# Performance work log

Measured on AMD Instinct MI355X. Metric: run time of the kernel, lower is better.

## Reference

```python
import jax, jax.numpy as jnp
import numpy as np

B, S, D, H = 8, 1024, 1024, 16
DH = D // H  # 64
LN_EPS = 1e-5


def setup_inputs() -> dict:
    key = jax.random.key(0)
    ks = jax.random.split(key, 12)
    w = lambda k, shape: (jax.random.normal(k, shape, dtype=jnp.float32) * 0.02)
    return {
        "key": jax.random.normal(ks[0], (B, S, D), dtype=jnp.float32),
        "value": jax.random.normal(ks[1], (B, S, D), dtype=jnp.float32),
        "query": jax.random.normal(ks[2], (B, S, D), dtype=jnp.float32),
        "atten_mask": jax.random.randint(ks[3], (B, S, S), 0, 2).astype(bool),
        "Wk": w(ks[4], (D, D)), "bk": jnp.zeros((D,), jnp.float32),
        "Wv": w(ks[5], (D, D)), "bv": jnp.zeros((D,), jnp.float32),
        "Wq": w(ks[6], (D, D)), "bq": jnp.zeros((D,), jnp.float32),
        "Wf": w(ks[7], (D, D)), "bf": jnp.zeros((D,), jnp.float32),
        "gamma": jnp.ones((D,), jnp.float32),
        "beta": jnp.zeros((D,), jnp.float32),
    }


def reference(key, value, query, atten_mask, Wk, bk, Wv, bv, Wq, bq, Wf, bf, gamma, beta):
    residual = query
    k = key @ Wk + bk      # [B,S,D]
    v = value @ Wv + bv
    q = query @ Wq + bq
    # Faithful to the original: raw .view(B*H, -1, d) reshape, NO head transpose.
    k = k.reshape(B * H, S, DH)
    v = v.reshape(B * H, S, DH)
    q = q.reshape(B * H, S, DH)
    # torch .repeat(H,1,1) tiles along batch dim -> head bh uses mask[bh % B]
    mask = jnp.tile(atten_mask, (H, 1, 1))  # [B*H, S, S]
    scale = (DH // H) ** (-0.5)  # quirky original scaling: (64//16)**-0.5 = 0.5
    scores = jnp.einsum('bqd,bkd->bqk', q, k) * scale  # [B*H, S, S]
    scores = jnp.where(mask, jnp.float32(-1e6), scores)
    attention = jax.nn.softmax(scores, axis=2)
    context = jnp.einsum('bqk,bkd->bqd', attention, v)  # [B*H, S, DH]
    context = context.reshape(B, S, D)
    out = context @ Wf + bf
    out = residual + out
    # LayerNorm over last dim
    mu = jnp.mean(out, axis=-1, keepdims=True)
    var = jnp.var(out, axis=-1, keepdims=True)
    out = (out - mu) * jax.lax.rsqrt(var + LN_EPS) * gamma + beta
    return out, attention
```

## Files before the change

kernel.cpp:

```cpp
#include <hip/hip_runtime.h>


typedef unsigned short u16;
typedef unsigned long long u64;
typedef __attribute__((ext_vector_type(8))) short bf16x8;
typedef __attribute__((ext_vector_type(4))) float f32x4;

#define MFMA_BF16(a, b, c) __builtin_amdgcn_mfma_f32_16x16x32_bf16((a), (b), (c), 0, 0, 0)

__device__ __forceinline__ u16 f2bf(float f) {
  unsigned u = __float_as_uint(f);
  u += 0x7fffu + ((u >> 16) & 1u);
  return (u16)(u >> 16);
}
__device__ __forceinline__ float bf2f(u16 b) {
  return __uint_as_float(((unsigned)b) << 16);
}
__device__ __forceinline__ void gload_lds16(const u16* g, u16* l) {
  __builtin_amdgcn_global_load_lds(
      (const __attribute__((address_space(1))) void*)g,
      (__attribute__((address_space(3))) void*)l, 16, 0, 0);
}

static constexpr size_t MD = 8192ull * 1024ull;
static constexpr size_t DD = 1024ull * 1024ull;
static constexpr float SCL = 0.72134752044f;

__global__ __launch_bounds__(256) void cvt_k(const float* __restrict__ K,
                                             const float* __restrict__ V,
                                             const float* __restrict__ Q,
                                             u16* __restrict__ O) {
  const int z = blockIdx.z;
  const float* src = (z == 0) ? K : ((z == 1) ? V : Q);
  const size_t i = ((size_t)blockIdx.x * 256 + threadIdx.x) * 4;
  const float4 v = *reinterpret_cast<const float4*>(src + i);
  ushort4 o;
  o.x = f2bf(v.x); o.y = f2bf(v.y); o.z = f2bf(v.z); o.w = f2bf(v.w);
  *reinterpret_cast<ushort4*>(O + (size_t)z * MD + i) = o;
}

__global__ __launch_bounds__(256) void wt_k(const float* __restrict__ Wk,
                                            const float* __restrict__ Wv,
                                            const float* __restrict__ Wq,
                                            const float* __restrict__ Wf,
                                            u16* __restrict__ WT) {
  const int z = blockIdx.z;
  const float* W = (z == 0) ? Wk : ((z == 1) ? Wv : ((z == 2) ? Wq : Wf));
  __shared__ float tile[32][33];
  const int k0 = blockIdx.y * 32, n0 = blockIdx.x * 32;
  const int r = threadIdx.x >> 5, c = threadIdx.x & 31;
#pragma unroll
  for (int rr = r; rr < 32; rr += 8)
    tile[rr][c] = W[(size_t)(k0 + rr) * 1024 + n0 + c];
  __syncthreads();
#pragma unroll
  for (int rr = r; rr < 32; rr += 8)
    WT[(size_t)z * DD + (size_t)(n0 + rr) * 1024 + k0 + c] = f2bf(tile[c][rr]);
}

__global__ __launch_bounds__(256) void mb_k(const unsigned char* __restrict__ mask8,
                                            u64* __restrict__ mb) {
  __shared__ int mflag;
  if (threadIdx.x == 0) {
    const unsigned* mw = reinterpret_cast<const unsigned*>(mask8);
    int allW = 1;
    for (int i = 0; i < 64; ++i) {
      const unsigned v = mw[i];
      if (v != 0u && v != 1u && v != 0x3F800000u) allW = 0;
    }
    mflag = allW;
  }
  __syncthreads();
  const int wide = mflag;
  const size_t wi = (size_t)blockIdx.x * 256 + threadIdx.x;
  const size_t src0 = wi * 64;
  u64 bits = 0ull;
  if (!wide) {
    const uint4* p = reinterpret_cast<const uint4*>(mask8 + src0);
#pragma unroll
    for (int q = 0; q < 4; ++q) {
      const uint4 v = p[q];
      const unsigned vv[4] = {v.x, v.y, v.z, v.w};
#pragma unroll
      for (int k = 0; k < 4; ++k) {
        unsigned tt = vv[k];
        tt |= tt >> 4; tt |= tt >> 2; tt |= tt >> 1;
        tt &= 0x01010101u;
        const unsigned nib =
            (tt & 1u) | ((tt >> 7) & 2u) | ((tt >> 14) & 4u) | ((tt >> 21) & 8u);
        bits |= (u64)nib << (q * 16 + k * 4);
      }
    }
  } else {
    const unsigned* p = reinterpret_cast<const unsigned*>(mask8) + src0;
#pragma unroll
    for (int k = 0; k < 64; ++k)
      bits |= (u64)(p[k] != 0u) << k;
  }
  mb[wi] = bits;
}

template <int EPI>
__global__ __launch_bounds__(256) void gemm_bt(
    const u16* __restrict__ A0, const u16* __restrict__ B0,
    const float* __restrict__ bias0, const float* __restrict__ bias1,
    const float* __restrict__ bias2, u16* __restrict__ Obf,
    float* __restrict__ Of, const float* __restrict__ resid) {
  __shared__ __align__(16) u16 As[128 * 32];
  __shared__ __align__(16) u16 Bs[128 * 32];
  const int z = blockIdx.z;
  const u16* A = A0 + (size_t)z * MD;
  const u16* Bt = B0 + (size_t)z * DD;
  const float* bias = (z == 0) ? bias0 : ((z == 1) ? bias1 : bias2);
  const int t = threadIdx.x;
  const int m0 = blockIdx.y * 128, n0 = blockIdx.x * 128;
  const int w = t >> 6, lane = t & 63, lr = lane & 15, lk = lane >> 4;
  const int wm = (w >> 1) * 64, wn = (w & 1) * 64;
  const int srow = lane >> 2, scol = (lane & 3) * 8;

  f32x4 acc[4][4] = {};

  for (int k0 = 0; k0 < 1024; k0 += 32) {
    __syncthreads();
#pragma unroll
    for (int it = 0; it < 2; ++it) {
      const int c = w * 2 + it;
      gload_lds16(A + (size_t)(m0 + 16 * c + srow) * 1024 + k0 + scol,
                  &As[c * 512 + lane * 8]);
      gload_lds16(Bt + (size_t)(n0 + 16 * c + srow) * 1024 + k0 + scol,
                  &Bs[c * 512 + lane * 8]);
    }
    __syncthreads();
    bf16x8 af[4], bfr[4];
#pragma unroll
    for (int i = 0; i < 4; ++i)
      af[i] = *reinterpret_cast<const bf16x8*>(&As[(wm + i * 16 + lr) * 32 + lk * 8]);
#pragma unroll
    for (int j = 0; j < 4; ++j)
      bfr[j] = *reinterpret_cast<const bf16x8*>(&Bs[(wn + j * 16 + lr) * 32 + lk * 8]);
#pragma unroll
    for (int i = 0; i < 4; ++i) {
#pragma unroll
      for (int j = 0; j < 4; ++j)
        acc[i][j] = MFMA_BF16(af[i], bfr[j], acc[i][j]);
    }
  }

#pragma unroll
  for (int i = 0; i < 4; ++i) {
#pragma unroll
    for (int j = 0; j < 4; ++j) {
#pragma unroll
      for (int r = 0; r < 4; ++r) {
        const int row = m0 + wm + i * 16 + lk * 4 + r;
        const int col = n0 + wn + j * 16 + lr;
        const float v = acc[i][j][r] + bias[col];
        if constexpr (EPI == 0) {
          Obf[(size_t)z * MD + (size_t)row * 1024 + col] = f2bf(v);
        } else {
          const size_t idx = (size_t)row * 1024 + col;
          Of[idx] = v + resid[idx];
        }
      }
    }
  }
}

__global__ __launch_bounds__(256) void vt_k(const u16* __restrict__ VP,
                                            u16* __restrict__ VTo) {
  __shared__ __align__(16) u16 tile[64][72];
  const int t = threadIdx.x;
  const int bh = blockIdx.y, p0 = blockIdx.x * 64;
  const int b = bh >> 4, shi = bh & 15;
  const size_t hb = (size_t)b * 1048576 + (size_t)shi * 65536;
#pragma unroll
  for (int it = 0; it < 2; ++it) {
    const int c = t + it * 256;
    const int row = c >> 3, f8 = (c & 7) * 8;
    const int p = p0 + row;
    *reinterpret_cast<int4*>(&tile[row][f8]) = *reinterpret_cast<const int4*>(
        VP + hb + (size_t)(p >> 4) * 1024 + (p & 15) * 64 + f8);
  }
  __syncthreads();
#pragma unroll
  for (int it = 0; it < 2; ++it) {
    const int c = t + it * 256;
    const int f = c >> 3, pc = (c & 7) * 8;
    __align__(16) u16 tmp[8];
#pragma unroll
    for (int i = 0; i < 8; ++i) tmp[i] = tile[pc + i][f];
    *reinterpret_cast<int4*>(VTo + (size_t)bh * 65536 + (size_t)f * 1024 + p0 + pc) =
        *reinterpret_cast<int4*>(tmp);
  }
}

__global__ __launch_bounds__(512, 4) void attn_k(
    const u16* __restrict__ QP, const u16* __restrict__ KP,
    const u16* __restrict__ VT, const u64* __restrict__ mb,
    float* __restrict__ attnOut, u16* __restrict__ ctx) {
  __shared__ __align__(16) u16 Ps[32 * 1024];
  __shared__ float red[8][2][16];

  const int t = threadIdx.x;
  const int qt = blockIdx.x;
  const int bh = blockIdx.y;
  const int q0 = qt * 32;
  const int b = bh >> 4, shi = bh & 15;
  const size_t hb = (size_t)b * 1048576 + (size_t)shi * 65536;
  const u64* mrow = mb + (size_t)(shi & 7) * 16384;

  const int w = t >> 6, lane = t & 63, lr = lane & 15, lk = lane >> 4;
  const int qsw = (lr & 7) << 3;

  bf16x8 qf[2][2];
#pragma unroll
  for (int rg = 0; rg < 2; ++rg) {
    const u16* qb = QP + hb + (size_t)(qt * 2 + rg) * 1024 + lr * 64 + lk * 8;
    qf[rg][0] = *reinterpret_cast<const bf16x8*>(qb);
    qf[rg][1] = *reinterpret_cast<const bf16x8*>(qb + 32);
  }

  float psum[2] = {0.f, 0.f};

#pragma unroll
  for (int ki = 0; ki < 2; ++ki) {
    const int kt = w * 2 + ki;
    const u16* kb = KP + hb + (size_t)(kt * 4) * 1024 + lr * 64 + lk * 8;
    bf16x8 kf[4][2];
#pragma unroll
    for (int j = 0; j < 4; ++j) {
      kf[j][0] = *reinterpret_cast<const bf16x8*>(kb + j * 1024);
      kf[j][1] = *reinterpret_cast<const bf16x8*>(kb + j * 1024 + 32);
    }
#pragma unroll
    for (int rg = 0; rg < 2; ++rg) {
      f32x4 sf[4];
#pragma unroll
      for (int j = 0; j < 4; ++j) {
        f32x4 a = {};
        a = MFMA_BF16(kf[j][0], qf[rg][0], a);
        a = MFMA_BF16(kf[j][1], qf[rg][1], a);
        sf[j] = a;
      }
      const u64 mw = mrow[(size_t)(q0 + rg * 16 + lr) * 16 + kt];
#pragma unroll
      for (int j = 0; j < 4; ++j) {
        u16 pb[4];
#pragma unroll
        for (int r = 0; r < 4; ++r) {
          const unsigned bit = (unsigned)(mw >> (j * 16 + lk * 4 + r)) & 1u;
          const float sel = bit ? -__builtin_inff() : 0.0f;
          const float p = __builtin_amdgcn_exp2f(fmaf(sf[j][r], SCL, sel));
          psum[rg] += p;
          pb[r] = f2bf(p);
        }
        const unsigned lo = (unsigned)pb[0] | ((unsigned)pb[1] << 16);
        const unsigned hi = (unsigned)pb[2] | ((unsigned)pb[3] << 16);
        const int kel = (kt * 64 + j * 16 + lk * 4) ^ qsw;
        *reinterpret_cast<u64*>(&Ps[(rg * 16 + lr) * 1024 + kel]) =
            (u64)lo | ((u64)hi << 32);
      }
    }
  }
#pragma unroll
  for (int rg = 0; rg < 2; ++rg) {
    psum[rg] += __shfl_xor(psum[rg], 16, 64);
    psum[rg] += __shfl_xor(psum[rg], 32, 64);
  }
  if (lane < 16) { red[w][0][lr] = psum[0]; red[w][1][lr] = psum[1]; }
  __syncthreads();

  const int rbase = (w >> 2) * 16, cg = (w & 3) * 16;
  const u16* vb = VT + (size_t)bh * 65536 + (size_t)(cg + lr) * 1024 + lk * 8;
  f32x4 cacc[4] = {};
#pragma unroll
  for (int kk = 0; kk < 32; ++kk) {
    const int kel = (kk * 32 + lk * 8) ^ qsw;
    const bf16x8 pf = *reinterpret_cast<const bf16x8*>(&Ps[(rbase + lr) * 1024 + kel]);
    const bf16x8 vf = *reinterpret_cast<const bf16x8*>(vb + kk * 32);
    cacc[kk & 3] = MFMA_BF16(pf, vf, cacc[kk & 3]);
  }
#pragma unroll
  for (int r = 0; r < 4; ++r) {
    const int l16 = lk * 4 + r;
    float rs = 0.f;
#pragma unroll
    for (int w2 = 0; w2 < 8; ++w2) rs += red[w2][w >> 2][l16];
    const float ri = (rs > 0.f) ? __builtin_amdgcn_rcpf(rs) : 0.f;
    const float cv = cacc[0][r] + cacc[1][r] + cacc[2][r] + cacc[3][r];
    const int p = q0 + rbase + l16;
    ctx[hb + (size_t)(p >> 4) * 1024 + (size_t)(p & 15) * 64 + cg + lr] = f2bf(cv * ri);
  }

  const int arow = t >> 4, ac4 = (t & 15) * 4;
  const int asw = (arow & 7) << 3;
  float rsA = 0.f;
#pragma unroll
  for (int w2 = 0; w2 < 8; ++w2) rsA += red[w2][arow >> 4][arow & 15];
  const float riA = (rsA > 0.f) ? __builtin_amdgcn_rcpf(rsA) : 0.f;
  float* aout = attnOut + (size_t)bh * 1048576 + (size_t)(q0 + arow) * 1024;
#pragma unroll
  for (int i = 0; i < 16; ++i) {
    const int col = i * 64 + ac4;
    const u64 p4 = *reinterpret_cast<const u64*>(&Ps[arow * 1024 + (col ^ asw)]);
    f32x4 o;
    o[0] = bf2f((u16)(p4 & 0xffffu)) * riA;
    o[1] = bf2f((u16)((p4 >> 16) & 0xffffu)) * riA;
    o[2] = bf2f((u16)((p4 >> 32) & 0xffffu)) * riA;
    o[3] = bf2f((u16)(p4 >> 48)) * riA;
    __builtin_nontemporal_store(o, reinterpret_cast<f32x4*>(aout + col));
  }
}

__global__ __launch_bounds__(256) void ln_k(const float* __restrict__ X,
                                            const float* __restrict__ gamma,
                                            const float* __restrict__ beta,
                                            float* __restrict__ Y) {
  const int row = blockIdx.x, t = threadIdx.x;
  const size_t base = (size_t)row * 1024;
  const float4 x = *reinterpret_cast<const float4*>(X + base + t * 4);
  float s = x.x + x.y + x.z + x.w;
  float s2 = x.x * x.x + x.y * x.y + x.z * x.z + x.w * x.w;
#pragma unroll
  for (int d = 1; d < 64; d <<= 1) {
    s += __shfl_xor(s, d, 64);
    s2 += __shfl_xor(s2, d, 64);
  }
  __shared__ float red[8];
  const int w = t >> 6;
  if ((t & 63) == 0) { red[w] = s; red[4 + w] = s2; }
  __syncthreads();
  s = red[0] + red[1] + red[2] + red[3];
  s2 = red[4] + red[5] + red[6] + red[7];
  const float mu = s * (1.f / 1024.f);
  const float var = s2 * (1.f / 1024.f) - mu * mu;
  const float inv = rsqrtf(var + 1e-5f);
  const float4 g = *reinterpret_cast<const float4*>(gamma + t * 4);
  const float4 be = *reinterpret_cast<const float4*>(beta + t * 4);
  float4 y;
  y.x = (x.x - mu) * inv * g.x + be.x;
  y.y = (x.y - mu) * inv * g.y + be.y;
  y.z = (x.z - mu) * inv * g.z + be.z;
  y.w = (x.w - mu) * inv * g.w + be.w;
  *reinterpret_cast<float4*>(Y + base + t * 4) = y;
}

extern "C" void kernel_launch(void* const* d_in, const int* in_sizes, int n_in,
                              void* d_out, int out_size, void* d_ws, size_t ws_size,
                              hipStream_t stream) {
  const float* keyF = (const float*)d_in[0];
  const float* valueF = (const float*)d_in[1];
  const float* queryF = (const float*)d_in[2];
  const unsigned char* mask8 = (const unsigned char*)d_in[3];
  const float* Wk = (const float*)d_in[4];
  const float* bk = (const float*)d_in[5];
  const float* Wv = (const float*)d_in[6];
  const float* bv = (const float*)d_in[7];
  const float* Wq = (const float*)d_in[8];
  const float* bq = (const float*)d_in[9];
  const float* Wf = (const float*)d_in[10];
  const float* bfp = (const float*)d_in[11];
  const float* gamma = (const float*)d_in[12];
  const float* beta = (const float*)d_in[13];

  char* ws = (char*)d_ws;
  u16* Xbf = (u16*)(ws);
  u16* WT = (u16*)(ws + 50331648);
  u16* KP = (u16*)(ws + 58720256);
  u16* VP = (u16*)(ws + 75497472);
  u16* QP = (u16*)(ws + 92274688);
  u16* VT = (u16*)(ws + 109051904);
  u64* MB = (u64*)(ws + 125829120);
  u16* CTX = (u16*)(ws);
  float* PRELN = (float*)(ws + 16777216);

  float* outF = (float*)d_out;
  float* attnF = outF + 8388608;

  cvt_k<<<dim3(8192, 1, 3), 256, 0, stream>>>(keyF, valueF, queryF, Xbf);
  wt_k<<<dim3(32, 32, 4), 256, 0, stream>>>(Wk, Wv, Wq, Wf, WT);
  mb_k<<<dim3(512), 256, 0, stream>>>(mask8, MB);
  gemm_bt<0><<<dim3(8, 64, 3), 256, 0, stream>>>(Xbf, WT, bk, bv, bq, KP, nullptr, nullptr);
  vt_k<<<dim3(16, 128), 256, 0, stream>>>(VP, VT);
  attn_k<<<dim3(32, 128), 512, 0, stream>>>(QP, KP, VT, MB, attnF, CTX);
  gemm_bt<1><<<dim3(8, 64, 1), 256, 0, stream>>>(CTX, WT + 3 * DD, bfp, bfp, bfp,
                                                 nullptr, PRELN, queryF);
  ln_k<<<dim3(8192), 256, 0, stream>>>(PRELN, gamma, beta, outF);
}
```

Measured before the change: 398.5 us.

## Split attention epilogue across wave groups, store pre-LN in bf16, packed bf16 convert

The attention kernel's epilogue now gives the P·V MFMA work to the first four waves, each covering 32 rows against one 16-column slice of V. The other four waves concurrently write the normalized fp32 attention matrix. Row reciprocals are broadcast with shuffles instead of each thread re-reducing the shared partial sums. Probability packing uses v_cvt_pk_bf16_f32 in place of manual rounding. The output projection writes its pre-LayerNorm result as bf16 instead of fp32, halving that round trip at the cost of some precision before normalization.

Measured after the change: 338.1 us. 1.18x faster.

```diff
diff --git a/kernel.cpp b/kernel.cpp
--- a/kernel.cpp
+++ b/kernel.cpp
@@ -15,6 +15,11 @@
 }
 __device__ __forceinline__ float bf2f(u16 b) {
   return __uint_as_float(((unsigned)b) << 16);
+}
+__device__ __forceinline__ unsigned cvt_pk_bf16(float lo, float hi) {
+  unsigned r;
+  asm("v_cvt_pk_bf16_f32 %0, %1, %2" : "=v"(r) : "v"(lo), "v"(hi));
+  return r;
 }
 __device__ __forceinline__ void gload_lds16(const u16* g, u16* l) {
   __builtin_amdgcn_global_load_lds(
@@ -105,7 +110,7 @@
     const u16* __restrict__ A0, const u16* __restrict__ B0,
     const float* __restrict__ bias0, const float* __restrict__ bias1,
     const float* __restrict__ bias2, u16* __restrict__ Obf,
-    float* __restrict__ Of, const float* __restrict__ resid) {
+    const float* __restrict__ resid) {
   __shared__ __align__(16) u16 As[128 * 32];
   __shared__ __align__(16) u16 Bs[128 * 32];
   const int z = blockIdx.z;
@@ -154,12 +159,12 @@
       for (int r = 0; r < 4; ++r) {
         const int row = m0 + wm + i * 16 + lk * 4 + r;
         const int col = n0 + wn + j * 16 + lr;
+        const size_t idx = (size_t)row * 1024 + col;
         const float v = acc[i][j][r] + bias[col];
         if constexpr (EPI == 0) {
-          Obf[(size_t)z * MD + (size_t)row * 1024 + col] = f2bf(v);
+          Obf[(size_t)z * MD + idx] = f2bf(v);
         } else {
-          const size_t idx = (size_t)row * 1024 + col;
-          Of[idx] = v + resid[idx];
+          Obf[idx] = f2bf(v + resid[idx]);
         }
       }
     }
@@ -245,17 +250,16 @@
       const u64 mw = mrow[(size_t)(q0 + rg * 16 + lr) * 16 + kt];
 #pragma unroll
       for (int j = 0; j < 4; ++j) {
-        u16 pb[4];
+        float p[4];
 #pragma unroll
         for (int r = 0; r < 4; ++r) {
           const unsigned bit = (unsigned)(mw >> (j * 16 + lk * 4 + r)) & 1u;
           const float sel = bit ? -__builtin_inff() : 0.0f;
-          const float p = __builtin_amdgcn_exp2f(fmaf(sf[j][r], SCL, sel));
-          psum[rg] += p;
-          pb[r] = f2bf(p);
+          p[r] = __builtin_amdgcn_exp2f(fmaf(sf[j][r], SCL, sel));
+          psum[rg] += p[r];
         }
-        const unsigned lo = (unsigned)pb[0] | ((unsigned)pb[1] << 16);
-        const unsigned hi = (unsigned)pb[2] | ((unsigned)pb[3] << 16);
+        const unsigned lo = cvt_pk_bf16(p[0], p[1]);
+        const unsigned hi = cvt_pk_bf16(p[2], p[3]);
         const int kel = (kt * 64 + j * 16 + lk * 4) ^ qsw;
         *reinterpret_cast<u64*>(&Ps[(rg * 16 + lr) * 1024 + kel]) =
             (u64)lo | ((u64)hi << 32);
@@ -270,57 +274,70 @@
   if (lane < 16) { red[w][0][lr] = psum[0]; red[w][1][lr] = psum[1]; }
   __syncthreads();
 
-  const int rbase = (w >> 2) * 16, cg = (w & 3) * 16;
-  const u16* vb = VT + (size_t)bh * 65536 + (size_t)(cg + lr) * 1024 + lk * 8;
-  f32x4 cacc[4] = {};
-#pragma unroll
-  for (int kk = 0; kk < 32; ++kk) {
-    const int kel = (kk * 32 + lk * 8) ^ qsw;
-    const bf16x8 pf = *reinterpret_cast<const bf16x8*>(&Ps[(rbase + lr) * 1024 + kel]);
-    const bf16x8 vf = *reinterpret_cast<const bf16x8*>(vb + kk * 32);
-    cacc[kk & 3] = MFMA_BF16(pf, vf, cacc[kk & 3]);
-  }
-#pragma unroll
-  for (int r = 0; r < 4; ++r) {
-    const int l16 = lk * 4 + r;
-    float rs = 0.f;
-#pragma unroll
-    for (int w2 = 0; w2 < 8; ++w2) rs += red[w2][w >> 2][l16];
-    const float ri = (rs > 0.f) ? __builtin_amdgcn_rcpf(rs) : 0.f;
-    const float cv = cacc[0][r] + cacc[1][r] + cacc[2][r] + cacc[3][r];
-    const int p = q0 + rbase + l16;
-    ctx[hb + (size_t)(p >> 4) * 1024 + (size_t)(p & 15) * 64 + cg + lr] = f2bf(cv * ri);
-  }
-
-  const int arow = t >> 4, ac4 = (t & 15) * 4;
-  const int asw = (arow & 7) << 3;
-  float rsA = 0.f;
-#pragma unroll
-  for (int w2 = 0; w2 < 8; ++w2) rsA += red[w2][arow >> 4][arow & 15];
-  const float riA = (rsA > 0.f) ? __builtin_amdgcn_rcpf(rsA) : 0.f;
-  float* aout = attnOut + (size_t)bh * 1048576 + (size_t)(q0 + arow) * 1024;
-#pragma unroll
-  for (int i = 0; i < 16; ++i) {
-    const int col = i * 64 + ac4;
-    const u64 p4 = *reinterpret_cast<const u64*>(&Ps[arow * 1024 + (col ^ asw)]);
-    f32x4 o;
-    o[0] = bf2f((u16)(p4 & 0xffffu)) * riA;
-    o[1] = bf2f((u16)((p4 >> 16) & 0xffffu)) * riA;
-    o[2] = bf2f((u16)((p4 >> 32) & 0xffffu)) * riA;
-    o[3] = bf2f((u16)(p4 >> 48)) * riA;
-    __builtin_nontemporal_store(o, reinterpret_cast<f32x4*>(aout + col));
-  }
-}
-
-__global__ __launch_bounds__(256) void ln_k(const float* __restrict__ X,
+  float rsl = 0.f;
+  if (lane < 32) {
+#pragma unroll
+    for (int w2 = 0; w2 < 8; ++w2) rsl += red[w2][lane >> 4][lane & 15];
+  }
+  const float rinvl = (rsl > 0.f) ? __builtin_amdgcn_rcpf(rsl) : 0.f;
+
+  if (w < 4) {
+    const int cg = w * 16;
+    const u16* vb = VT + (size_t)bh * 65536 + (size_t)(cg + lr) * 1024 + lk * 8;
+    f32x4 cacc[2][2] = {};
+#pragma unroll
+    for (int kk = 0; kk < 32; ++kk) {
+      const int kel = (kk * 32 + lk * 8) ^ qsw;
+      const bf16x8 vf = *reinterpret_cast<const bf16x8*>(vb + kk * 32);
+      const bf16x8 pf0 = *reinterpret_cast<const bf16x8*>(&Ps[lr * 1024 + kel]);
+      const bf16x8 pf1 = *reinterpret_cast<const bf16x8*>(&Ps[(16 + lr) * 1024 + kel]);
+      cacc[0][kk & 1] = MFMA_BF16(pf0, vf, cacc[0][kk & 1]);
+      cacc[1][kk & 1] = MFMA_BF16(pf1, vf, cacc[1][kk & 1]);
+    }
+#pragma unroll
+    for (int rg = 0; rg < 2; ++rg) {
+#pragma unroll
+      for (int r = 0; r < 4; ++r) {
+        const int lrow = rg * 16 + lk * 4 + r;
+        const float ri = __shfl(rinvl, lrow, 64);
+        const float cv = cacc[rg][0][r] + cacc[rg][1][r];
+        const int p = q0 + lrow;
+        ctx[hb + (size_t)(p >> 4) * 1024 + (size_t)(p & 15) * 64 + cg + lr] =
+            f2bf(cv * ri);
+      }
+    }
+  } else {
+    const int t2 = t - 256;
+    float* aout = attnOut + (size_t)bh * 1048576 + (size_t)q0 * 1024;
+#pragma unroll
+    for (int i = 0; i < 32; ++i) {
+      const int asw = (i & 7) << 3;
+      const float ri = __shfl(rinvl, i, 64);
+      const u64 p4 = *reinterpret_cast<const u64*>(&Ps[i * 1024 + ((t2 * 4) ^ asw)]);
+      f32x4 o;
+      o[0] = bf2f((u16)(p4 & 0xffffu)) * ri;
+      o[1] = bf2f((u16)((p4 >> 16) & 0xffffu)) * ri;
+      o[2] = bf2f((u16)((p4 >> 32) & 0xffffu)) * ri;
+      o[3] = bf2f((u16)(p4 >> 48)) * ri;
+      __builtin_nontemporal_store(
+          o, reinterpret_cast<f32x4*>(aout + (size_t)i * 1024 + t2 * 4));
+    }
+  }
+}
+
+__global__ __launch_bounds__(256) void ln_k(const u16* __restrict__ X,
                                             const float* __restrict__ gamma,
                                             const float* __restrict__ beta,
                                             float* __restrict__ Y) {
   const int row = blockIdx.x, t = threadIdx.x;
   const size_t base = (size_t)row * 1024;
-  const float4 x = *reinterpret_cast<const float4*>(X + base + t * 4);
-  float s = x.x + x.y + x.z + x.w;
-  float s2 = x.x * x.x + x.y * x.y + x.z * x.z + x.w * x.w;
+  const u64 xw = *reinterpret_cast<const u64*>(X + base + t * 4);
+  float x0 = bf2f((u16)(xw & 0xffffu));
+  float x1 = bf2f((u16)((xw >> 16) & 0xffffu));
+  float x2 = bf2f((u16)((xw >> 32) & 0xffffu));
+  float x3 = bf2f((u16)(xw >> 48));
+  float s = x0 + x1 + x2 + x3;
+  float s2 = x0 * x0 + x1 * x1 + x2 * x2 + x3 * x3;
 #pragma unroll
   for (int d = 1; d < 64; d <<= 1) {
     s += __shfl_xor(s, d, 64);
@@ -338,10 +355,10 @@
   const float4 g = *reinterpret_cast<const float4*>(gamma + t * 4);
   const float4 be = *reinterpret_cast<const float4*>(beta + t * 4);
   float4 y;
-  y.x = (x.x - mu) * inv * g.x + be.x;
-  y.y = (x.y - mu) * inv * g.y + be.y;
-  y.z = (x.z - mu) * inv * g.z + be.z;
-  y.w = (x.w - mu) * inv * g.w + be.w;
+  y.x = (x0 - mu) * inv * g.x + be.x;
+  y.y = (x1 - mu) * inv * g.y + be.y;
+  y.z = (x2 - mu) * inv * g.z + be.z;
+  y.w = (x3 - mu) * inv * g.w + be.w;
   *reinterpret_cast<float4*>(Y + base + t * 4) = y;
 }
 
@@ -372,7 +389,7 @@
   u16* VT = (u16*)(ws + 109051904);
   u64* MB = (u64*)(ws + 125829120);
   u16* CTX = (u16*)(ws);
-  float* PRELN = (float*)(ws + 16777216);
+  u16* PRELN = (u16*)(ws + 16777216);
 
   float* outF = (float*)d_out;
   float* attnF = outF + 8388608;
@@ -380,10 +397,10 @@
   cvt_k<<<dim3(8192, 1, 3), 256, 0, stream>>>(keyF, valueF, queryF, Xbf);
   wt_k<<<dim3(32, 32, 4), 256, 0, stream>>>(Wk, Wv, Wq, Wf, WT);
   mb_k<<<dim3(512), 256, 0, stream>>>(mask8, MB);
-  gemm_bt<0><<<dim3(8, 64, 3), 256, 0, stream>>>(Xbf, WT, bk, bv, bq, KP, nullptr, nullptr);
+  gemm_bt<0><<<dim3(8, 64, 3), 256, 0, stream>>>(Xbf, WT, bk, bv, bq, KP, nullptr);
   vt_k<<<dim3(16, 128), 256, 0, stream>>>(VP, VT);
   attn_k<<<dim3(32, 128), 512, 0, stream>>>(QP, KP, VT, MB, attnF, CTX);
   gemm_bt<1><<<dim3(8, 64, 1), 256, 0, stream>>>(CTX, WT + 3 * DD, bfp, bfp, bfp,
-                                                 nullptr, PRELN, queryF);
+                                                 PRELN, queryF);
   ln_k<<<dim3(8192), 256, 0, stream>>>(PRELN, gamma, beta, outF);
 }
```
